# Kernel tuning notes

Measured on AMD Instinct MI355X. Metric: run time of the kernel, lower is better.

Reference implementation:

```python
import jax, jax.numpy as jnp
import numpy as np

B, S, D = 4, 2048, 1024
H, HD = 16, 64  # heads, head_dim; H*HD == D


def setup_inputs() -> dict:
    key = jax.random.key(0)
    k_x, k_qkv, k_proj = jax.random.split(key, 3)
    x = jax.random.normal(k_x, (B, S, D), dtype=jnp.float32)
    # init scale ~ 1/sqrt(fan_in) to keep activations sane
    w_qkv = jax.random.normal(k_qkv, (D, 3 * H * HD), dtype=jnp.float32) / np.sqrt(D)
    b_qkv = jnp.zeros((3 * H * HD,), dtype=jnp.float32)
    w_proj = jax.random.normal(k_proj, (H * HD, D), dtype=jnp.float32) / np.sqrt(H * HD)
    b_proj = jnp.zeros((D,), dtype=jnp.float32)
    return {"x": x, "w_qkv": w_qkv, "b_qkv": b_qkv, "w_proj": w_proj,
            "b_proj": b_proj, "layer_idx": 0}


def reference(x, w_qkv, b_qkv, w_proj, b_proj, layer_idx):
    # c_attn: [B,S,D] -> [B,S,3*H*HD]
    qkv = x @ w_qkv + b_qkv
    qkv = qkv.reshape(B, S, 3, H, HD)
    q, k, v = qkv[:, :, 0], qkv[:, :, 1], qkv[:, :, 2]  # each [B,S,H,HD]

    scale = jax.lax.rsqrt(float(HD))  # scale_by_inverse_layer_idx=False
    # scores: [B,H,S_q,S_k]
    scores = jnp.einsum("bqhd,bkhd->bhqk", q, k) * scale
    causal = jnp.tril(jnp.ones((S, S), dtype=jnp.bool_))
    scores = jnp.where(causal, scores, -1e9)
    attn = jax.nn.softmax(scores, axis=-1)  # dropout is identity (inference)

    out = jnp.einsum("bhqk,bkhd->bqhd", attn, v).reshape(B, S, H * HD)
    return out @ w_proj + b_proj
```

## Files before the change

kernel.cpp:

```cpp
#include <hip/hip_runtime.h>

typedef __attribute__((ext_vector_type(8))) short short8;
typedef __attribute__((ext_vector_type(4))) float f32x4;
typedef __attribute__((ext_vector_type(16))) float f32x16;
typedef __attribute__((ext_vector_type(4))) float flt4;
typedef __attribute__((ext_vector_type(4))) unsigned int u32x4;
typedef unsigned short bfbits;

#define DEVI __device__ __forceinline__

constexpr int Bc = 4, Sc = 2048, Dc = 1024, Hc = 16, HDc = 64;
constexpr int M1 = Bc * Sc;
constexpr int N1 = 3 * Hc * HDc;
constexpr int Kd = Dc;
constexpr float QSCALE = 0.125f * 1.4426950408889634f;
constexpr float MSHIFT = 12.0f;

typedef __attribute__((address_space(1))) const unsigned int gas_u32;
typedef __attribute__((address_space(3))) unsigned int las_u32;

DEVI void gld_lds16(const void* g, void* l) {
  __builtin_amdgcn_global_load_lds((gas_u32*)g, (las_u32*)l, 16, 0, 0);
}

DEVI unsigned short f2bf(float f) {
  unsigned int x = __builtin_bit_cast(unsigned int, f);
  x = x + 0x7fffu + ((x >> 16) & 1u);
  return (unsigned short)(x >> 16);
}

DEVI f32x4 zero4() { f32x4 z = {0.f, 0.f, 0.f, 0.f}; return z; }

DEVI short8 lds8(const void* base, int byteoff) {
  return *(const short8*)((const char*)base + byteoff);
}

DEVI unsigned int cvtpk_bf16(float lo, float hi) {
  unsigned int r;
  asm("v_cvt_pk_bf16_f32 %0, %1, %2" : "=v"(r) : "v"(lo), "v"(hi));
  return r;
}

DEVI void pl32swap(unsigned int& dst, unsigned int& src) {
  asm volatile("v_permlane32_swap_b32 %0, %1" : "+v"(dst), "+v"(src));
}

__global__ void cast_x_kernel(const float* __restrict__ in, bfbits* __restrict__ out, int n8) {
  int i = blockIdx.x * 256 + threadIdx.x;
  if (i >= n8) return;
  const flt4* p = (const flt4*)in;
  flt4 a = p[(size_t)2 * i];
  flt4 b = p[(size_t)2 * i + 1];
  short8 r;
  r[0] = (short)f2bf(a[0]); r[1] = (short)f2bf(a[1]);
  r[2] = (short)f2bf(a[2]); r[3] = (short)f2bf(a[3]);
  r[4] = (short)f2bf(b[0]); r[5] = (short)f2bf(b[1]);
  r[6] = (short)f2bf(b[2]); r[7] = (short)f2bf(b[3]);
  *(short8*)(out + (size_t)8 * i) = r;
}

__global__ void transpose_cast_kernel(const float* __restrict__ in, bfbits* __restrict__ out,
                                      int R, int C) {
  __shared__ float tile[32][33];
  int bc = blockIdx.x * 32, br = blockIdx.y * 32;
  int tx = threadIdx.x & 31, ty = threadIdx.x >> 5;
#pragma unroll
  for (int i = 0; i < 32; i += 8)
    tile[ty + i][tx] = in[(size_t)(br + ty + i) * C + bc + tx];
  __syncthreads();
#pragma unroll
  for (int i = 0; i < 32; i += 8)
    out[(size_t)(bc + ty + i) * R + br + tx] = f2bf(tile[tx][ty + i]);
}

template <int EPI>
__global__ __launch_bounds__(256, 2) void gemm_bt_kernel(
    const bfbits* __restrict__ A, const bfbits* __restrict__ Bt,
    const float* __restrict__ bias,
    bfbits* __restrict__ outQ, bfbits* __restrict__ outK, bfbits* __restrict__ outV,
    float* __restrict__ outF, int M, int N, int K, int nbase) {
  __shared__ bfbits sA[128 * 64];
  __shared__ bfbits sB[128 * 64];
  const int t = threadIdx.x;
  const int wid = t >> 6, l = t & 63;
  const int lr = l & 15, lg = l >> 4;
  const int m0 = blockIdx.y * 128, n0 = nbase + blockIdx.x * 128;
  const int wr = (wid >> 1) * 64, wc = (wid & 1) * 64;

  f32x4 acc[4][4];
#pragma unroll
  for (int i = 0; i < 4; ++i)
#pragma unroll
    for (int j = 0; j < 4; ++j) acc[i][j] = zero4();

  const int row_s = t >> 3;
  const int grp_s = t & 7;

  for (int kt = 0; kt < K; kt += 64) {
#pragma unroll
    for (int i = 0; i < 4; ++i) {
      int row = i * 32 + row_s;
      int grp = grp_s ^ (row & 7);
      gld_lds16(A + (size_t)(m0 + row) * K + kt + grp * 8, sA + i * 2048 + wid * 512);
      gld_lds16(Bt + (size_t)(n0 + row) * K + kt + grp * 8, sB + i * 2048 + wid * 512);
    }
    __syncthreads();
#pragma unroll
    for (int ks = 0; ks < 2; ++ks) {
      short8 af[4], bf[4];
#pragma unroll
      for (int i = 0; i < 4; ++i) {
        int rA = wr + i * 16 + lr;
        af[i] = lds8(sA, rA * 128 + (((ks * 4 + lg) ^ (rA & 7)) << 4));
        int rB = wc + i * 16 + lr;
        bf[i] = lds8(sB, rB * 128 + (((ks * 4 + lg) ^ (rB & 7)) << 4));
      }
#pragma unroll
      for (int i = 0; i < 4; ++i)
#pragma unroll
        for (int j = 0; j < 4; ++j) {
          if (EPI == 2)
            acc[i][j] = __builtin_amdgcn_mfma_f32_16x16x32_bf16(bf[j], af[i], acc[i][j], 0, 0, 0);
          else
            acc[i][j] = __builtin_amdgcn_mfma_f32_16x16x32_bf16(af[i], bf[j], acc[i][j], 0, 0, 0);
        }
    }
    __syncthreads();
  }

#pragma unroll
  for (int i = 0; i < 4; ++i) {
#pragma unroll
    for (int j = 0; j < 4; ++j) {
#pragma unroll
      for (int r = 0; r < 4; ++r) {
        if (EPI == 2) {
          int c = n0 + wc + j * 16 + lg * 4 + r;
          int m = m0 + wr + i * 16 + lr;
          float v = acc[i][j][r] + bias[c];
          int h = (c >> 6) & 15, d = c & 63;
          int b = m >> 11, s = m & 2047;
          outV[((size_t)(b * 16 + h) * 64 + d) * 2048 + s] = f2bf(v);
        } else {
          int row = m0 + wr + i * 16 + lg * 4 + r;
          int col = n0 + wc + j * 16 + lr;
          float v = acc[i][j][r] + bias[col];
          if (EPI == 0) {
            int h = (col >> 6) & 15;
            int d = col & 63;
            int b = row >> 11;
            int s = row & 2047;
            if ((col >> 10) == 0)
              outQ[((size_t)(b * 16 + h) * 2048 + s) * 64 + d] = f2bf(v * QSCALE);
            else
              outK[((size_t)(b * 16 + h) * 2048 + s) * 64 + d] = f2bf(v);
          } else {
            outF[(size_t)row * N + col] = v;
          }
        }
      }
    }
  }
}

__global__ __launch_bounds__(256, 2) void attn_kernel(
    const bfbits* __restrict__ Q, const bfbits* __restrict__ K,
    const bfbits* __restrict__ Vt, bfbits* __restrict__ O) {
  __shared__ bfbits sK[2 * 64 * 64];
  __shared__ bfbits sV[2 * 64 * 64];

  const int t = threadIdx.x, wid = t >> 6, l = t & 63;
  const int lq = l & 31, b5 = l >> 5;

  const int id = blockIdx.x;
  const int swz = (id & 7) * 64 + (id >> 3);
  const int pr = swz & 7;
  const int bh = swz >> 3;
  const int b = bh >> 4, h = bh & 15;

  const bfbits* Qb = Q + (size_t)bh * Sc * HDc;
  const bfbits* Kb = K + (size_t)bh * Sc * HDc;
  const bfbits* Vtb = Vt + (size_t)bh * Sc * HDc;

  const int row_s = t >> 3, grp_s = t & 7;

  auto STAGE = [&](int kb, int bufi) {
    const int kv0s = kb * 64;
#pragma unroll
    for (int i = 0; i < 2; ++i) {
      int rr = i * 32 + row_s;
      int grp = grp_s ^ (rr & 7);
      gld_lds16(Kb + (size_t)(kv0s + rr) * 64 + grp * 8,
                sK + bufi * 4096 + i * 2048 + wid * 512);
      gld_lds16(Vtb + (size_t)rr * Sc + kv0s + grp * 8,
                sV + bufi * 4096 + i * 2048 + wid * 512);
    }
  };

  for (int half = 0; half < 2; ++half) {
    const int qt = half ? (15 - pr) : pr;
    const int qb = qt * 128;
    const int qrow = qb + wid * 32 + lq;
    const int qmaxw = qb + wid * 32 + 31;

    short8 qf[4];
#pragma unroll
    for (int ds = 0; ds < 4; ++ds)
      qf[ds] = *(const short8*)(Qb + (size_t)qrow * 64 + ds * 16 + b5 * 8);

    f32x16 acc0 = {0.f, 0.f, 0.f, 0.f, 0.f, 0.f, 0.f, 0.f,
                   0.f, 0.f, 0.f, 0.f, 0.f, 0.f, 0.f, 0.f};
    f32x16 acc1 = acc0;
    float lrow = 0.f;

    const int nkv = 2 * (qt + 1);
    int cur = 0;
    STAGE(0, 0);
    __syncthreads();

    for (int kb = 0; kb < nkv; ++kb) {
      const int kv0 = kb * 64;
      if (kb + 1 < nkv) STAGE(kb + 1, cur ^ 1);
      const bfbits* bK = sK + cur * 4096;
      const bfbits* bV = sV + cur * 4096;

#pragma unroll
      for (int sub = 0; sub < 2; ++sub) {
        const int kvb = kv0 + sub * 32;
        if (kvb <= qmaxw) {
          f32x16 st = {0.f, 0.f, 0.f, 0.f, 0.f, 0.f, 0.f, 0.f,
                       0.f, 0.f, 0.f, 0.f, 0.f, 0.f, 0.f, 0.f};
          const int rK = sub * 32 + lq;
          const int swK = rK & 7;
          __builtin_amdgcn_s_setprio(1);
#pragma unroll
          for (int ds = 0; ds < 4; ++ds) {
            short8 kf = lds8(bK, rK * 128 + (((ds * 2 + b5) ^ swK) << 4));
            st = __builtin_amdgcn_mfma_f32_32x32x16_bf16(kf, qf[ds], st, 0, 0, 0);
          }
          __builtin_amdgcn_s_setprio(0);
          if (kvb + 31 > qb + wid * 32) {
#pragma unroll
            for (int r = 0; r < 16; ++r) {
              int kvi = kvb + (r & 3) + 8 * (r >> 2) + 4 * b5;
              st[r] = (kvi > qrow) ? -1e30f : st[r];
            }
          }
          float ssum = 0.f;
#pragma unroll
          for (int r = 0; r < 16; ++r) {
            float p = exp2f(st[r] - MSHIFT);
            st[r] = p;
            ssum += p;
          }
          lrow += ssum;
          unsigned int W0 = cvtpk_bf16(st[0], st[1]);
          unsigned int W1 = cvtpk_bf16(st[2], st[3]);
          unsigned int W2 = cvtpk_bf16(st[4], st[5]);
          unsigned int W3 = cvtpk_bf16(st[6], st[7]);
          unsigned int W4 = cvtpk_bf16(st[8], st[9]);
          unsigned int W5 = cvtpk_bf16(st[10], st[11]);
          unsigned int W6 = cvtpk_bf16(st[12], st[13]);
          unsigned int W7 = cvtpk_bf16(st[14], st[15]);
          pl32swap(W0, W2);
          pl32swap(W1, W3);
          pl32swap(W4, W6);
          pl32swap(W5, W7);
          u32x4 pa0u = {W0, W1, W2, W3};
          u32x4 pa1u = {W4, W5, W6, W7};
          short8 pa0 = __builtin_bit_cast(short8, pa0u);
          short8 pa1 = __builtin_bit_cast(short8, pa1u);
          __builtin_amdgcn_s_setprio(1);
#pragma unroll
          for (int dt = 0; dt < 2; ++dt) {
            int rv = dt * 32 + lq;
            int swV = rv & 7;
            short8 vf0 = lds8(bV, rv * 128 + (((sub * 4 + 0 + b5) ^ swV) << 4));
            short8 vf1 = lds8(bV, rv * 128 + (((sub * 4 + 2 + b5) ^ swV) << 4));
            if (dt == 0) {
              acc0 = __builtin_amdgcn_mfma_f32_32x32x16_bf16(pa0, vf0, acc0, 0, 0, 0);
              acc0 = __builtin_amdgcn_mfma_f32_32x32x16_bf16(pa1, vf1, acc0, 0, 0, 0);
            } else {
              acc1 = __builtin_amdgcn_mfma_f32_32x32x16_bf16(pa0, vf0, acc1, 0, 0, 0);
              acc1 = __builtin_amdgcn_mfma_f32_32x32x16_bf16(pa1, vf1, acc1, 0, 0, 0);
            }
          }
          __builtin_amdgcn_s_setprio(0);
        }
      }
      __syncthreads();
      cur ^= 1;
    }

    float lsum = lrow + __shfl_xor(lrow, 32);
    float inv = 1.0f / lsum;
#pragma unroll
    for (int r = 0; r < 16; ++r) {
      int qrel = (r & 3) + 8 * (r >> 2) + 4 * b5;
      float ib = __shfl(inv, qrel, 32);
      int srow = qb + wid * 32 + qrel;
      size_t base = (size_t)(b * Sc + srow) * (Hc * HDc) + h * 64;
      O[base + lq] = f2bf(acc0[r] * ib);
      O[base + 32 + lq] = f2bf(acc1[r] * ib);
    }
  }
}

extern "C" void kernel_launch(void* const* d_in, const int* in_sizes, int n_in,
                              void* d_out, int out_size, void* d_ws, size_t ws_size,
                              hipStream_t stream) {
  const float* x = (const float*)d_in[0];
  const float* w_qkv = (const float*)d_in[1];
  const float* b_qkv = (const float*)d_in[2];
  const float* w_proj = (const float*)d_in[3];
  const float* b_proj = (const float*)d_in[4];
  float* out = (float*)d_out;

  char* ws = (char*)d_ws;
  size_t off = 0;
  auto alloc = [&](size_t bytes) {
    char* p = ws + off;
    off = off + ((bytes + 255) & ~(size_t)255);
    return p;
  };
  bfbits* Xb = (bfbits*)alloc((size_t)M1 * Kd * 2);
  bfbits* WqkvT = (bfbits*)alloc((size_t)N1 * Kd * 2);
  bfbits* WprojT = (bfbits*)alloc((size_t)Dc * Dc * 2);
  bfbits* Qb = (bfbits*)alloc((size_t)Bc * Hc * Sc * HDc * 2);
  bfbits* Kb = (bfbits*)alloc((size_t)Bc * Hc * Sc * HDc * 2);
  bfbits* Vtb = (bfbits*)alloc((size_t)Bc * Hc * Sc * HDc * 2);
  bfbits* Ob = Xb;

  cast_x_kernel<<<(M1 * Kd / 8 + 255) / 256, 256, 0, stream>>>(x, Xb, M1 * Kd / 8);
  transpose_cast_kernel<<<dim3(N1 / 32, Kd / 32), 256, 0, stream>>>(w_qkv, WqkvT, Kd, N1);
  transpose_cast_kernel<<<dim3(Dc / 32, Dc / 32), 256, 0, stream>>>(w_proj, WprojT, Dc, Dc);

  gemm_bt_kernel<0><<<dim3(16, M1 / 128), 256, 0, stream>>>(
      Xb, WqkvT, b_qkv, Qb, Kb, nullptr, nullptr, M1, N1, Kd, 0);
  gemm_bt_kernel<2><<<dim3(8, M1 / 128), 256, 0, stream>>>(
      Xb, WqkvT, b_qkv, nullptr, nullptr, Vtb, nullptr, M1, N1, Kd, 2048);

  attn_kernel<<<dim3(512), 256, 0, stream>>>(Qb, Kb, Vtb, Ob);

  gemm_bt_kernel<1><<<dim3(Dc / 128, M1 / 128), 256, 0, stream>>>(
      Ob, WprojT, b_proj, nullptr, nullptr, nullptr, out, M1, Dc, Kd, 0);
}
```

Measured before the change: 276.2 us.

## Merge QKV GEMM launches, split attention per q-tile, compute row sums via MFMA

Folds the separate V-transpose GEMM launch into the main QKV GEMM by picking the operand order and epilogue per block at runtime. The attention kernel now launches one block per 128-row query tile (1024 blocks) instead of pairing light and heavy tiles inside one block, and occupancy hints are raised for both kernels. The softmax shift is folded into the initial score accumulator, and row sums come from an extra MFMA against a ones vector instead of scalar adds plus shuffles. The aim is less launch and ALU overhead and more parallelism, at the risk of causal load imbalance across blocks and register pressure from the higher occupancy targets.

```diff
diff --git a/kernel.cpp b/kernel.cpp
--- a/kernel.cpp
+++ b/kernel.cpp
@@ -74,18 +74,19 @@
 }
 
 template <int EPI>
-__global__ __launch_bounds__(256, 2) void gemm_bt_kernel(
+__global__ __launch_bounds__(256, 3) void gemm_bt_kernel(
     const bfbits* __restrict__ A, const bfbits* __restrict__ Bt,
     const float* __restrict__ bias,
     bfbits* __restrict__ outQ, bfbits* __restrict__ outK, bfbits* __restrict__ outV,
-    float* __restrict__ outF, int M, int N, int K, int nbase) {
+    float* __restrict__ outF, int M, int N, int K) {
   __shared__ bfbits sA[128 * 64];
   __shared__ bfbits sB[128 * 64];
   const int t = threadIdx.x;
   const int wid = t >> 6, l = t & 63;
   const int lr = l & 15, lg = l >> 4;
-  const int m0 = blockIdx.y * 128, n0 = nbase + blockIdx.x * 128;
+  const int m0 = blockIdx.y * 128, n0 = blockIdx.x * 128;
   const int wr = (wid >> 1) * 64, wc = (wid & 1) * 64;
+  const bool swapop = (EPI == 0) && (n0 >= 2048);
 
   f32x4 acc[4][4];
 #pragma unroll
@@ -115,15 +116,19 @@
         int rB = wc + i * 16 + lr;
         bf[i] = lds8(sB, rB * 128 + (((ks * 4 + lg) ^ (rB & 7)) << 4));
       }
-#pragma unroll
-      for (int i = 0; i < 4; ++i)
-#pragma unroll
-        for (int j = 0; j < 4; ++j) {
-          if (EPI == 2)
+      if (swapop) {
+#pragma unroll
+        for (int i = 0; i < 4; ++i)
+#pragma unroll
+          for (int j = 0; j < 4; ++j)
             acc[i][j] = __builtin_amdgcn_mfma_f32_16x16x32_bf16(bf[j], af[i], acc[i][j], 0, 0, 0);
-          else
+      } else {
+#pragma unroll
+        for (int i = 0; i < 4; ++i)
+#pragma unroll
+          for (int j = 0; j < 4; ++j)
             acc[i][j] = __builtin_amdgcn_mfma_f32_16x16x32_bf16(af[i], bf[j], acc[i][j], 0, 0, 0);
-        }
+      }
     }
     __syncthreads();
   }
@@ -134,7 +139,7 @@
     for (int j = 0; j < 4; ++j) {
 #pragma unroll
       for (int r = 0; r < 4; ++r) {
-        if (EPI == 2) {
+        if (EPI == 0 && n0 >= 2048) {
           int c = n0 + wc + j * 16 + lg * 4 + r;
           int m = m0 + wr + i * 16 + lr;
           float v = acc[i][j][r] + bias[c];
@@ -163,7 +168,7 @@
   }
 }
 
-__global__ __launch_bounds__(256, 2) void attn_kernel(
+__global__ __launch_bounds__(256, 4) void attn_kernel(
     const bfbits* __restrict__ Q, const bfbits* __restrict__ K,
     const bfbits* __restrict__ Vt, bfbits* __restrict__ O) {
   __shared__ bfbits sK[2 * 64 * 64];
@@ -173,9 +178,9 @@
   const int lq = l & 31, b5 = l >> 5;
 
   const int id = blockIdx.x;
-  const int swz = (id & 7) * 64 + (id >> 3);
-  const int pr = swz & 7;
-  const int bh = swz >> 3;
+  const int swz = (id & 7) * 128 + (id >> 3);
+  const int qt = swz & 15;
+  const int bh = swz >> 4;
   const int b = bh >> 4, h = bh & 15;
 
   const bfbits* Qb = Q + (size_t)bh * Sc * HDc;
@@ -197,112 +202,107 @@
     }
   };
 
-  for (int half = 0; half < 2; ++half) {
-    const int qt = half ? (15 - pr) : pr;
-    const int qb = qt * 128;
-    const int qrow = qb + wid * 32 + lq;
-    const int qmaxw = qb + wid * 32 + 31;
-
-    short8 qf[4];
-#pragma unroll
-    for (int ds = 0; ds < 4; ++ds)
-      qf[ds] = *(const short8*)(Qb + (size_t)qrow * 64 + ds * 16 + b5 * 8);
-
-    f32x16 acc0 = {0.f, 0.f, 0.f, 0.f, 0.f, 0.f, 0.f, 0.f,
-                   0.f, 0.f, 0.f, 0.f, 0.f, 0.f, 0.f, 0.f};
-    f32x16 acc1 = acc0;
-    float lrow = 0.f;
-
-    const int nkv = 2 * (qt + 1);
-    int cur = 0;
-    STAGE(0, 0);
+  const int qb = qt * 128;
+  const int qrow = qb + wid * 32 + lq;
+  const int qmaxw = qb + wid * 32 + 31;
+
+  short8 qf[4];
+#pragma unroll
+  for (int ds = 0; ds < 4; ++ds)
+    qf[ds] = *(const short8*)(Qb + (size_t)qrow * 64 + ds * 16 + b5 * 8);
+
+  short8 onesf;
+#pragma unroll
+  for (int j = 0; j < 8; ++j) onesf[j] = (short)0x3F80;
+
+  f32x16 acc0 = {0.f, 0.f, 0.f, 0.f, 0.f, 0.f, 0.f, 0.f,
+                 0.f, 0.f, 0.f, 0.f, 0.f, 0.f, 0.f, 0.f};
+  f32x16 acc1 = acc0;
+  f32x16 accS = acc0;
+
+  const int nkv = 2 * (qt + 1);
+  int cur = 0;
+  STAGE(0, 0);
+  __syncthreads();
+
+  for (int kb = 0; kb < nkv; ++kb) {
+    const int kv0 = kb * 64;
+    if (kb + 1 < nkv) STAGE(kb + 1, cur ^ 1);
+    const bfbits* bK = sK + cur * 4096;
+    const bfbits* bV = sV + cur * 4096;
+
+#pragma unroll
+    for (int sub = 0; sub < 2; ++sub) {
+      const int kvb = kv0 + sub * 32;
+      if (kvb <= qmaxw) {
+        f32x16 st = {-MSHIFT, -MSHIFT, -MSHIFT, -MSHIFT, -MSHIFT, -MSHIFT, -MSHIFT, -MSHIFT,
+                     -MSHIFT, -MSHIFT, -MSHIFT, -MSHIFT, -MSHIFT, -MSHIFT, -MSHIFT, -MSHIFT};
+        const int rK = sub * 32 + lq;
+        const int swK = rK & 7;
+        __builtin_amdgcn_s_setprio(1);
+#pragma unroll
+        for (int ds = 0; ds < 4; ++ds) {
+          short8 kf = lds8(bK, rK * 128 + (((ds * 2 + b5) ^ swK) << 4));
+          st = __builtin_amdgcn_mfma_f32_32x32x16_bf16(kf, qf[ds], st, 0, 0, 0);
+        }
+        __builtin_amdgcn_s_setprio(0);
+        if (kvb + 31 > qb + wid * 32) {
+#pragma unroll
+          for (int r = 0; r < 16; ++r) {
+            int kvi = kvb + (r & 3) + 8 * (r >> 2) + 4 * b5;
+            st[r] = (kvi > qrow) ? -1e30f : st[r];
+          }
+        }
+#pragma unroll
+        for (int r = 0; r < 16; ++r) st[r] = exp2f(st[r]);
+        unsigned int W0 = cvtpk_bf16(st[0], st[1]);
+        unsigned int W1 = cvtpk_bf16(st[2], st[3]);
+        unsigned int W2 = cvtpk_bf16(st[4], st[5]);
+        unsigned int W3 = cvtpk_bf16(st[6], st[7]);
+        unsigned int W4 = cvtpk_bf16(st[8], st[9]);
+        unsigned int W5 = cvtpk_bf16(st[10], st[11]);
+        unsigned int W6 = cvtpk_bf16(st[12], st[13]);
+        unsigned int W7 = cvtpk_bf16(st[14], st[15]);
+        pl32swap(W0, W2);
+        pl32swap(W1, W3);
+        pl32swap(W4, W6);
+        pl32swap(W5, W7);
+        u32x4 pa0u = {W0, W1, W2, W3};
+        u32x4 pa1u = {W4, W5, W6, W7};
+        short8 pa0 = __builtin_bit_cast(short8, pa0u);
+        short8 pa1 = __builtin_bit_cast(short8, pa1u);
+        __builtin_amdgcn_s_setprio(1);
+#pragma unroll
+        for (int dt = 0; dt < 2; ++dt) {
+          int rv = dt * 32 + lq;
+          int swV = rv & 7;
+          short8 vf0 = lds8(bV, rv * 128 + (((sub * 4 + 0 + b5) ^ swV) << 4));
+          short8 vf1 = lds8(bV, rv * 128 + (((sub * 4 + 2 + b5) ^ swV) << 4));
+          if (dt == 0) {
+            acc0 = __builtin_amdgcn_mfma_f32_32x32x16_bf16(pa0, vf0, acc0, 0, 0, 0);
+            acc0 = __builtin_amdgcn_mfma_f32_32x32x16_bf16(pa1, vf1, acc0, 0, 0, 0);
+          } else {
+            acc1 = __builtin_amdgcn_mfma_f32_32x32x16_bf16(pa0, vf0, acc1, 0, 0, 0);
+            acc1 = __builtin_amdgcn_mfma_f32_32x32x16_bf16(pa1, vf1, acc1, 0, 0, 0);
+          }
+        }
+        accS = __builtin_amdgcn_mfma_f32_32x32x16_bf16(pa0, onesf, accS, 0, 0, 0);
+        accS = __builtin_amdgcn_mfma_f32_32x32x16_bf16(pa1, onesf, accS, 0, 0, 0);
+        __builtin_amdgcn_s_setprio(0);
+      }
+    }
     __syncthreads();
-
-    for (int kb = 0; kb < nkv; ++kb) {
-      const int kv0 = kb * 64;
-      if (kb + 1 < nkv) STAGE(kb + 1, cur ^ 1);
-      const bfbits* bK = sK + cur * 4096;
-      const bfbits* bV = sV + cur * 4096;
-
-#pragma unroll
-      for (int sub = 0; sub < 2; ++sub) {
-        const int kvb = kv0 + sub * 32;
-        if (kvb <= qmaxw) {
-          f32x16 st = {0.f, 0.f, 0.f, 0.f, 0.f, 0.f, 0.f, 0.f,
-                       0.f, 0.f, 0.f, 0.f, 0.f, 0.f, 0.f, 0.f};
-          const int rK = sub * 32 + lq;
-          const int swK = rK & 7;
-          __builtin_amdgcn_s_setprio(1);
-#pragma unroll
-          for (int ds = 0; ds < 4; ++ds) {
-            short8 kf = lds8(bK, rK * 128 + (((ds * 2 + b5) ^ swK) << 4));
-            st = __builtin_amdgcn_mfma_f32_32x32x16_bf16(kf, qf[ds], st, 0, 0, 0);
-          }
-          __builtin_amdgcn_s_setprio(0);
-          if (kvb + 31 > qb + wid * 32) {
-#pragma unroll
-            for (int r = 0; r < 16; ++r) {
-              int kvi = kvb + (r & 3) + 8 * (r >> 2) + 4 * b5;
-              st[r] = (kvi > qrow) ? -1e30f : st[r];
-            }
-          }
-          float ssum = 0.f;
-#pragma unroll
-          for (int r = 0; r < 16; ++r) {
-            float p = exp2f(st[r] - MSHIFT);
-            st[r] = p;
-            ssum += p;
-          }
-          lrow += ssum;
-          unsigned int W0 = cvtpk_bf16(st[0], st[1]);
-          unsigned int W1 = cvtpk_bf16(st[2], st[3]);
-          unsigned int W2 = cvtpk_bf16(st[4], st[5]);
-          unsigned int W3 = cvtpk_bf16(st[6], st[7]);
-          unsigned int W4 = cvtpk_bf16(st[8], st[9]);
-          unsigned int W5 = cvtpk_bf16(st[10], st[11]);
-          unsigned int W6 = cvtpk_bf16(st[12], st[13]);
-          unsigned int W7 = cvtpk_bf16(st[14], st[15]);
-          pl32swap(W0, W2);
-          pl32swap(W1, W3);
-          pl32swap(W4, W6);
-          pl32swap(W5, W7);
-          u32x4 pa0u = {W0, W1, W2, W3};
-          u32x4 pa1u = {W4, W5, W6, W7};
-          short8 pa0 = __builtin_bit_cast(short8, pa0u);
-          short8 pa1 = __builtin_bit_cast(short8, pa1u);
-          __builtin_amdgcn_s_setprio(1);
-#pragma unroll
-          for (int dt = 0; dt < 2; ++dt) {
-            int rv = dt * 32 + lq;
-            int swV = rv & 7;
-            short8 vf0 = lds8(bV, rv * 128 + (((sub * 4 + 0 + b5) ^ swV) << 4));
-            short8 vf1 = lds8(bV, rv * 128 + (((sub * 4 + 2 + b5) ^ swV) << 4));
-            if (dt == 0) {
-              acc0 = __builtin_amdgcn_mfma_f32_32x32x16_bf16(pa0, vf0, acc0, 0, 0, 0);
-              acc0 = __builtin_amdgcn_mfma_f32_32x32x16_bf16(pa1, vf1, acc0, 0, 0, 0);
-            } else {
-              acc1 = __builtin_amdgcn_mfma_f32_32x32x16_bf16(pa0, vf0, acc1, 0, 0, 0);
-              acc1 = __builtin_amdgcn_mfma_f32_32x32x16_bf16(pa1, vf1, acc1, 0, 0, 0);
-            }
-          }
-          __builtin_amdgcn_s_setprio(0);
-        }
-      }
-      __syncthreads();
-      cur ^= 1;
-    }
-
-    float lsum = lrow + __shfl_xor(lrow, 32);
-    float inv = 1.0f / lsum;
-#pragma unroll
-    for (int r = 0; r < 16; ++r) {
-      int qrel = (r & 3) + 8 * (r >> 2) + 4 * b5;
-      float ib = __shfl(inv, qrel, 32);
-      int srow = qb + wid * 32 + qrel;
-      size_t base = (size_t)(b * Sc + srow) * (Hc * HDc) + h * 64;
-      O[base + lq] = f2bf(acc0[r] * ib);
-      O[base + 32 + lq] = f2bf(acc1[r] * ib);
-    }
+    cur ^= 1;
+  }
+
+#pragma unroll
+  for (int r = 0; r < 16; ++r) {
+    float ib = 1.0f / accS[r];
+    int qrel = (r & 3) + 8 * (r >> 2) + 4 * b5;
+    int srow = qb + wid * 32 + qrel;
+    size_t base = (size_t)(b * Sc + srow) * (Hc * HDc) + h * 64;
+    O[base + lq] = f2bf(acc0[r] * ib);
+    O[base + 32 + lq] = f2bf(acc1[r] * ib);
   }
 }
 
@@ -335,13 +335,11 @@
   transpose_cast_kernel<<<dim3(N1 / 32, Kd / 32), 256, 0, stream>>>(w_qkv, WqkvT, Kd, N1);
   transpose_cast_kernel<<<dim3(Dc / 32, Dc / 32), 256, 0, stream>>>(w_proj, WprojT, Dc, Dc);
 
-  gemm_bt_kernel<0><<<dim3(16, M1 / 128), 256, 0, stream>>>(
-      Xb, WqkvT, b_qkv, Qb, Kb, nullptr, nullptr, M1, N1, Kd, 0);
-  gemm_bt_kernel<2><<<dim3(8, M1 / 128), 256, 0, stream>>>(
-      Xb, WqkvT, b_qkv, nullptr, nullptr, Vtb, nullptr, M1, N1, Kd, 2048);
-
-  attn_kernel<<<dim3(512), 256, 0, stream>>>(Qb, Kb, Vtb, Ob);
+  gemm_bt_kernel<0><<<dim3(N1 / 128, M1 / 128), 256, 0, stream>>>(
+      Xb, WqkvT, b_qkv, Qb, Kb, Vtb, nullptr, M1, N1, Kd);
+
+  attn_kernel<<<dim3(1024), 256, 0, stream>>>(Qb, Kb, Vtb, Ob);
 
   gemm_bt_kernel<1><<<dim3(Dc / 128, M1 / 128), 256, 0, stream>>>(
-      Ob, WprojT, b_proj, nullptr, nullptr, nullptr, out, M1, Dc, Kd, 0);
-}
+      Ob, WprojT, b_proj, nullptr, nullptr, nullptr, out, M1, Dc, Kd);
+}
```

New measurement: 488.8 us. +77.0%, slower.
